# Optimization experiments

Measured on AMD Instinct MI355X. Metric: run time of the kernel, lower is better.

The kernel has to match this reference:

```python
import jax, jax.numpy as jnp
import numpy as np

N = 5000        # nodes (repo uses 'sample/5000')
D_IN = 512      # feature dim
D_OUT = 16      # output_dim
K = 3           # num meta-paths
N_CLASSES = 100 # num_Labels
P_EDGE = 0.0064 # ~32 avg degree


def setup_inputs() -> dict:
    key = jax.random.key(0)
    ks = jax.random.split(key, 8)
    features = jax.random.normal(ks[0], (N, D_IN), dtype=jnp.float32)
    # sparse binary similarity matrices, symmetrized
    adj = (jax.random.uniform(ks[1], (K, N, N)) < P_EDGE).astype(jnp.float32)
    adj = jnp.maximum(adj, adj.transpose(0, 2, 1))
    W_gnn = jax.random.normal(ks[2], (K, D_IN, D_OUT), dtype=jnp.float32) / np.sqrt(D_IN).astype(np.float32)
    b_gnn = jnp.zeros((K, D_OUT), dtype=jnp.float32)
    att_w = jax.random.normal(ks[3], (K, 2 * D_OUT, 1), dtype=jnp.float32)  # as in torch.randn
    W_final = jax.random.normal(ks[4], (D_OUT, N_CLASSES), dtype=jnp.float32) / np.sqrt(D_OUT).astype(np.float32)
    b_final = jnp.zeros((N_CLASSES,), dtype=jnp.float32)
    return dict(features=features, adj=adj, W_gnn=W_gnn, b_gnn=b_gnn,
                att_w=att_w, W_final=W_final, b_final=b_final)


def _gcn_norm(A_bin):
    # GCNConv normalization: D^{-1/2} (A + I) D^{-1/2} with unit edge weights
    n = A_bin.shape[-1]
    Ahat = A_bin + jnp.eye(n, dtype=A_bin.dtype)
    dinv = jax.lax.rsqrt(Ahat.sum(-1))  # deg >= 1 due to self loops
    return dinv[..., :, None] * Ahat * dinv[..., None, :]


def reference(features, adj, W_gnn, b_gnn, att_w, W_final, b_final):
    # --- per-meta-path GCNConv (edge weights are all 1, from nonzero pattern) ---
    norm = _gcn_norm((adj != 0).astype(features.dtype))          # [K,N,N]
    XW = jnp.einsum('nd,kdo->kno', features, W_gnn)              # [K,N,Dout]
    h = jnp.einsum('knm,kmo->kno', norm, XW) + b_gnn[:, None, :]
    f_meta = jnp.max(h, axis=0)                                  # 'max' aggregation, [N,Dout]

    # --- pairwise attention over meta-paths (vectorized NxN loop) ---
    d = f_meta.shape[1]
    a = f_meta @ att_w[:, :d, 0].T   # [N,K] contribution of f_meta[i]
    b = f_meta @ att_w[:, d:, 0].T   # [N,K] contribution of f_meta[j]
    scores = jnp.exp(jax.nn.relu(a[:, None, :] + b[None, :, :]))  # [N,N,K]
    attn = scores / scores.sum(-1, keepdims=True)

    # --- fuse meta-path adjacencies ---
    A_meta = jnp.einsum('nmk,knm->nm', attn, adj)                # [N,N]

    # --- final GCNConv on the nonzero pattern of A_meta (unit edge weights) ---
    norm_meta = _gcn_norm((A_meta != 0).astype(features.dtype))
    predictions = norm_meta @ (f_meta @ W_final) + b_final
    return f_meta, A_meta, predictions
```

## Files before the change

kernel.cpp:

```cpp
#include <hip/hip_runtime.h>
#include <cstdint>
#include <cstddef>

#define N_NODES 5000
#define DIN 512
#define DOUT 16
#define KMP 3
#define NCLS 100
#define WSTRIDE 160
#define NWORDS 157
#define NQ 1250
#define CAPK 160
#define CAPU 320
#define NJT 313
#define NXW (KMP * NJT)

typedef float f32x4 __attribute__((ext_vector_type(4)));

__global__ __launch_bounds__(256)
void kA(const float* __restrict__ adj, const float* __restrict__ feat,
        const float* __restrict__ Wg,
        uint32_t* __restrict__ planes, float* __restrict__ dinv,
        float* __restrict__ udinv,
        uint16_t* __restrict__ nbrK, int* __restrict__ cntK,
        uint16_t* __restrict__ nbrU, int* __restrict__ cntU,
        float* __restrict__ XW) {
    int bid = blockIdx.x;
    int t = threadIdx.x;

    if (bid >= N_NODES) {
        int b2 = bid - N_NODES;
        int k = b2 / NJT;
        int jt = b2 - k * NJT;
        int j = jt * 16 + (t >> 4);
        int o = t & 15;
        if (j < N_NODES) {
            const float4* f4 = (const float4*)(feat + (size_t)j * DIN);
            const float* wk = Wg + (size_t)k * DIN * DOUT + o;
            float acc = 0.f;
            #pragma unroll 4
            for (int d4 = 0; d4 < DIN / 4; ++d4) {
                float4 f = f4[d4];
                acc += f.x * wk[(4 * d4 + 0) * DOUT]
                     + f.y * wk[(4 * d4 + 1) * DOUT]
                     + f.z * wk[(4 * d4 + 2) * DOUT]
                     + f.w * wk[(4 * d4 + 3) * DOUT];
            }
            XW[((size_t)k * N_NODES + j) * DOUT + o] = acc;
        }
        return;
    }

    int i = bid;
    int lane = t & 63;
    int wv   = t >> 6;
    __shared__ uint32_t nib32[KMP][320];
    __shared__ int wtot[4][4];

    #pragma unroll
    for (int it = 0; it < 15; ++it) {
        const int k  = it / 5;
        const int ql = (it - 5 * k) * 256 + t;
        uint32_t m = 0;
        if (ql < NQ) {
            const f32x4* arow4 = (const f32x4*)(adj + ((size_t)k * N_NODES + i) * N_NODES);
            f32x4 v = __builtin_nontemporal_load(arow4 + ql);
            m = (v.x != 0.f ? 1u : 0u) | (v.y != 0.f ? 2u : 0u) |
                (v.z != 0.f ? 4u : 0u) | (v.w != 0.f ? 8u : 0u);
        }
        ((uint8_t*)nib32[k])[ql] = (uint8_t)m;
    }
    __syncthreads();

    uint32_t w[4];
    int cnt[4];
    #pragma unroll
    for (int k = 0; k < KMP; ++k) {
        uint32_t word = 0;
        if (t < NWORDS) {
            uint32_t lo = nib32[k][2 * t], hi = nib32[k][2 * t + 1];
            word = (lo & 0xFu) | ((lo >> 4) & 0xF0u) | ((lo >> 8) & 0xF00u) | ((lo >> 12) & 0xF000u)
                 | ((hi << 16) & 0xF0000u) | ((hi << 12) & 0xF00000u)
                 | ((hi << 8) & 0xF000000u) | ((hi << 4) & 0xF0000000u);
            planes[((size_t)k * N_NODES + i) * WSTRIDE + t] = word;
        }
        w[k] = word;
        cnt[k] = __popc(word);
    }
    w[3] = w[0] | w[1] | w[2];
    cnt[3] = __popc(w[3]);

    int x[4];
    #pragma unroll
    for (int q = 0; q < 4; ++q) x[q] = cnt[q];
    #pragma unroll
    for (int s = 1; s < 64; s <<= 1) {
        int y0 = __shfl_up(x[0], s), y1 = __shfl_up(x[1], s);
        int y2 = __shfl_up(x[2], s), y3 = __shfl_up(x[3], s);
        if (lane >= s) { x[0] += y0; x[1] += y1; x[2] += y2; x[3] += y3; }
    }
    if (lane == 63) {
        wtot[0][wv] = x[0]; wtot[1][wv] = x[1];
        wtot[2][wv] = x[2]; wtot[3][wv] = x[3];
    }
    __syncthreads();

    #pragma unroll
    for (int q = 0; q < 4; ++q) {
        int prefix = 0, total = 0;
        #pragma unroll
        for (int wq = 0; wq < 4; ++wq) {
            int v = wtot[q][wq];
            total += v;
            if (wq < wv) prefix += v;
        }
        int pos = prefix + x[q] - cnt[q];
        uint32_t word = w[q];
        if (q < KMP) {
            uint16_t* out = nbrK + ((size_t)q * N_NODES + i) * CAPK;
            while (word) {
                int b = __builtin_ctz(word);
                word &= word - 1;
                if (pos < CAPK) out[pos] = (uint16_t)(32 * t + b);
                ++pos;
            }
            if (t == 0) {
                dinv[q * N_NODES + i] = rsqrtf(1.0f + (float)total);
                cntK[q * N_NODES + i] = (total < CAPK) ? total : CAPK;
            }
        } else {
            uint16_t* out = nbrU + (size_t)i * CAPU;
            while (word) {
                int b = __builtin_ctz(word);
                word &= word - 1;
                if (pos < CAPU) out[pos] = (uint16_t)(32 * t + b);
                ++pos;
            }
            if (t == 0) {
                cntU[i] = (total < CAPU) ? total : CAPU;
                udinv[i] = rsqrtf(1.0f + (float)total);
            }
        }
    }
}

__global__ __launch_bounds__(256)
void k34_fmeta_ab_gd(const uint16_t* __restrict__ nbrK, const int* __restrict__ cntK,
                     const float* __restrict__ XW, const float* __restrict__ dinv,
                     const float* __restrict__ bg, const float* __restrict__ aw,
                     const float* __restrict__ Wf, const float* __restrict__ udinv,
                     float* __restrict__ f_meta, float* __restrict__ a4,
                     float* __restrict__ b4, float* __restrict__ Gd) {
    int t = threadIdx.x;
    int wv = t >> 6;
    int lane = t & 63;
    int o = lane & 15;
    int s = lane >> 4;
    int i = blockIdx.x * 4 + wv;
    __shared__ float fs[4][17];

    float hmax = -1e30f;
    #pragma unroll
    for (int k = 0; k < KMP; ++k) {
        const float* xw = XW + (size_t)k * N_NODES * DOUT;
        const float* dv = dinv + (size_t)k * N_NODES;
        int row = k * N_NODES + i;
        int nn = cntK[row];
        const uint16_t* nb = nbrK + (size_t)row * CAPK;
        float di = dv[i];
        float a0 = 0.f, a1 = 0.f, a2 = 0.f, a3 = 0.f;
        for (int n0 = 4 * s; n0 < nn; n0 += 16) {
            ushort4 jj = *(const ushort4*)(nb + n0);
            a0 += dv[jj.x] * xw[(int)jj.x * DOUT + o];
            if (n0 + 1 < nn) a1 += dv[jj.y] * xw[(int)jj.y * DOUT + o];
            if (n0 + 2 < nn) a2 += dv[jj.z] * xw[(int)jj.z * DOUT + o];
            if (n0 + 3 < nn) a3 += dv[jj.w] * xw[(int)jj.w * DOUT + o];
        }
        float red = (a0 + a1) + (a2 + a3);
        red += __shfl_xor(red, 16);
        red += __shfl_xor(red, 32);
        red += di * xw[i * DOUT + o];
        float h = di * red + bg[k * DOUT + o];
        hmax = fmaxf(hmax, h);
    }
    if (s == 0) {
        f_meta[i * DOUT + o] = hmax;
        fs[wv][o] = hmax;
    }
    __syncthreads();

    float sa0 = hmax * aw[0 * 32 + o], sb0 = hmax * aw[0 * 32 + 16 + o];
    float sa1 = hmax * aw[1 * 32 + o], sb1 = hmax * aw[1 * 32 + 16 + o];
    float sa2 = hmax * aw[2 * 32 + o], sb2 = hmax * aw[2 * 32 + 16 + o];
    #pragma unroll
    for (int sh = 1; sh < 16; sh <<= 1) {
        sa0 += __shfl_xor(sa0, sh, 16); sb0 += __shfl_xor(sb0, sh, 16);
        sa1 += __shfl_xor(sa1, sh, 16); sb1 += __shfl_xor(sb1, sh, 16);
        sa2 += __shfl_xor(sa2, sh, 16); sb2 += __shfl_xor(sb2, sh, 16);
    }
    if (s == 0 && o < 4) {
        float sa = (o == 0) ? sa0 : (o == 1) ? sa1 : (o == 2) ? sa2 : 0.f;
        float sb = (o == 0) ? sb0 : (o == 1) ? sb1 : (o == 2) ? sb2 : 0.f;
        a4[i * 4 + o] = sa;
        b4[i * 4 + o] = sb;
    }

    float f[DOUT];
    #pragma unroll
    for (int q = 0; q < DOUT; ++q) f[q] = fs[wv][q];
    float ud = udinv[i];
    for (int c = lane; c < NCLS; c += 64) {
        float acc = 0.f;
        #pragma unroll
        for (int q = 0; q < DOUT; ++q) acc += f[q] * Wf[q * NCLS + c];
        Gd[(size_t)i * NCLS + c] = acc * ud;
    }
}

__device__ __forceinline__ float attn_frac(float x0, float x1, float x2,
                                           uint32_t b0, uint32_t b1, uint32_t b2) {
    float e0 = __expf(fmaxf(x0, 0.f));
    float e1 = __expf(fmaxf(x1, 0.f));
    float e2 = __expf(fmaxf(x2, 0.f));
    float num = (b0 ? e0 : 0.f) + (b1 ? e1 : 0.f) + (b2 ? e2 : 0.f);
    return __fdividef(num, e0 + e1 + e2);
}

#define NB_K5 625

__global__ __launch_bounds__(256)
void kC(const uint32_t* __restrict__ planes,
        const float* __restrict__ a4, const float* __restrict__ b4,
        float* __restrict__ Am,
        const uint16_t* __restrict__ nbrU, const int* __restrict__ cntU,
        const float* __restrict__ Gd, const float* __restrict__ udinv,
        const float* __restrict__ bf, float* __restrict__ pred) {
    int bid = blockIdx.x;
    int t = threadIdx.x;

    if (bid < NB_K5) {
        int i0 = bid * 8;
        __shared__ float a_s[8][3];
        if (t < 24) { int r = t / 3, k = t % 3; a_s[r][k] = a4[(i0 + r) * 4 + k]; }
        __syncthreads();
        for (int c = 0; c < 5; ++c) {
            int j4 = 4 * (t + 256 * c);
            if (j4 >= N_NODES) break;
            int w = j4 >> 5, sh = j4 & 31;
            const float4* bp = (const float4*)(b4 + (size_t)j4 * 4);
            float4 bj0 = bp[0], bj1 = bp[1], bj2 = bp[2], bj3 = bp[3];
            #pragma unroll
            for (int r = 0; r < 8; ++r) {
                int i = i0 + r;
                uint32_t q0 = planes[(size_t)i * WSTRIDE + w] >> sh;
                uint32_t q1 = planes[(size_t)(N_NODES + i) * WSTRIDE + w] >> sh;
                uint32_t q2 = planes[(size_t)(2 * N_NODES + i) * WSTRIDE + w] >> sh;
                uint32_t un = (q0 | q1 | q2) & 0xFu;
                f32x4 outv = (f32x4)(0.f);
                if (un) {
                    float A0 = a_s[r][0], A1 = a_s[r][1], A2 = a_s[r][2];
                    if (un & 1u) outv.x = attn_frac(A0 + bj0.x, A1 + bj0.y, A2 + bj0.z, q0 & 1u, q1 & 1u, q2 & 1u);
                    if (un & 2u) outv.y = attn_frac(A0 + bj1.x, A1 + bj1.y, A2 + bj1.z, q0 & 2u, q1 & 2u, q2 & 2u);
                    if (un & 4u) outv.z = attn_frac(A0 + bj2.x, A1 + bj2.y, A2 + bj2.z, q0 & 4u, q1 & 4u, q2 & 4u);
                    if (un & 8u) outv.w = attn_frac(A0 + bj3.x, A1 + bj3.y, A2 + bj3.z, q0 & 8u, q1 & 8u, q2 & 8u);
                }
                __builtin_nontemporal_store(outv, (f32x4*)(Am + (size_t)i * N_NODES + j4));
            }
        }
    } else {
        int b2 = bid - NB_K5;
        int i = b2 * 2 + (t >> 7);
        int c = t & 127;
        if (c >= NCLS) return;
        int nn = cntU[i];
        const uint16_t* nb = nbrU + (size_t)i * CAPU;
        float a0 = Gd[(size_t)i * NCLS + c];
        float a1 = 0.f, a2 = 0.f, a3 = 0.f;
        int n = 0;
        for (; n + 4 <= nn; n += 4) {
            ushort4 jj = *(const ushort4*)(nb + n);
            a0 += Gd[(size_t)jj.x * NCLS + c];
            a1 += Gd[(size_t)jj.y * NCLS + c];
            a2 += Gd[(size_t)jj.z * NCLS + c];
            a3 += Gd[(size_t)jj.w * NCLS + c];
        }
        for (; n < nn; ++n) a0 += Gd[(size_t)nb[n] * NCLS + c];
        pred[(size_t)i * NCLS + c] = udinv[i] * ((a0 + a1) + (a2 + a3)) + bf[c];
    }
}

extern "C" void kernel_launch(void* const* d_in, const int* in_sizes, int n_in,
                              void* d_out, int out_size, void* d_ws, size_t ws_size,
                              hipStream_t stream) {
    const float* feat = (const float*)d_in[0];
    const float* adj  = (const float*)d_in[1];
    const float* Wg   = (const float*)d_in[2];
    const float* bg   = (const float*)d_in[3];
    const float* aw   = (const float*)d_in[4];
    const float* Wf   = (const float*)d_in[5];
    const float* bf   = (const float*)d_in[6];

    float* f_meta = (float*)d_out;
    float* Am     = f_meta + (size_t)N_NODES * DOUT;
    float* pred   = Am + (size_t)N_NODES * N_NODES;

    char* ws = (char*)d_ws;
    size_t off = 0;
    auto alloc = [&](size_t bytes) {
        void* p = ws + off;
        off = (off + bytes + 255) & ~(size_t)255;
        return p;
    };
    uint32_t* planes = (uint32_t*)alloc((size_t)KMP * N_NODES * WSTRIDE * 4);
    float* dinv  = (float*)alloc((size_t)KMP * N_NODES * 4);
    float* XW    = (float*)alloc((size_t)KMP * N_NODES * DOUT * 4);
    float* a4    = (float*)alloc((size_t)N_NODES * 16);
    float* b4    = (float*)alloc((size_t)N_NODES * 16);
    float* udinv = (float*)alloc((size_t)N_NODES * 4);
    float* Gd    = (float*)alloc((size_t)N_NODES * NCLS * 4);
    uint16_t* nbrK = (uint16_t*)alloc((size_t)KMP * N_NODES * CAPK * 2);
    int*      cntK = (int*)alloc((size_t)KMP * N_NODES * 4);
    uint16_t* nbrU = (uint16_t*)alloc((size_t)N_NODES * CAPU * 2);
    int*      cntU = (int*)alloc((size_t)N_NODES * 4);

    hipLaunchKernelGGL(kA, dim3(N_NODES + NXW), dim3(256), 0, stream,
                       adj, feat, Wg, planes, dinv, udinv, nbrK, cntK, nbrU, cntU, XW);
    hipLaunchKernelGGL(k34_fmeta_ab_gd, dim3(N_NODES / 4), dim3(256), 0, stream,
                       nbrK, cntK, XW, dinv, bg, aw, Wf, udinv, f_meta, a4, b4, Gd);
    hipLaunchKernelGGL(kC, dim3(NB_K5 + N_NODES / 2), dim3(256), 0, stream,
                       planes, a4, b4, Am, nbrU, cntU, Gd, udinv, bf, pred);
}
```

Baseline: 532.1 us.

## Rebalance work splits across XW, f_meta and A_meta kernels

The XW projection blocks now compute all three meta-paths per block, so each feature row is loaded once instead of three times, and the XW grid is a third the size. The f_meta kernel now uses one block per node with one wave per meta-path, combining results through shared memory instead of looping over meta-paths serially in a single wave. The A_meta kernel processes 4 rows per block instead of 8, doubling the block count. These changes trade redundant loads and serial loops for more parallelism, at the cost of extra blocks and more b4 reloads in the attention kernel.

```diff
diff --git a/kernel.cpp b/kernel.cpp
--- a/kernel.cpp
+++ b/kernel.cpp
@@ -13,7 +13,6 @@
 #define CAPK 160
 #define CAPU 320
 #define NJT 313
-#define NXW (KMP * NJT)
 
 typedef float f32x4 __attribute__((ext_vector_type(4)));
 
@@ -30,23 +29,28 @@
 
     if (bid >= N_NODES) {
         int b2 = bid - N_NODES;
-        int k = b2 / NJT;
-        int jt = b2 - k * NJT;
-        int j = jt * 16 + (t >> 4);
+        int j = b2 * 16 + (t >> 4);
         int o = t & 15;
         if (j < N_NODES) {
-            const float4* f4 = (const float4*)(feat + (size_t)j * DIN);
-            const float* wk = Wg + (size_t)k * DIN * DOUT + o;
-            float acc = 0.f;
-            #pragma unroll 4
+            const f32x4* f4 = (const f32x4*)(feat + (size_t)j * DIN);
+            const float* w0 = Wg + (size_t)0 * DIN * DOUT + o;
+            const float* w1 = Wg + (size_t)1 * DIN * DOUT + o;
+            const float* w2 = Wg + (size_t)2 * DIN * DOUT + o;
+            float acc0 = 0.f, acc1 = 0.f, acc2 = 0.f;
+            #pragma unroll 2
             for (int d4 = 0; d4 < DIN / 4; ++d4) {
-                float4 f = f4[d4];
-                acc += f.x * wk[(4 * d4 + 0) * DOUT]
-                     + f.y * wk[(4 * d4 + 1) * DOUT]
-                     + f.z * wk[(4 * d4 + 2) * DOUT]
-                     + f.w * wk[(4 * d4 + 3) * DOUT];
-            }
-            XW[((size_t)k * N_NODES + j) * DOUT + o] = acc;
+                f32x4 f = f4[d4];
+                int d = 4 * d4;
+                acc0 += f.x * w0[(d + 0) * DOUT] + f.y * w0[(d + 1) * DOUT]
+                      + f.z * w0[(d + 2) * DOUT] + f.w * w0[(d + 3) * DOUT];
+                acc1 += f.x * w1[(d + 0) * DOUT] + f.y * w1[(d + 1) * DOUT]
+                      + f.z * w1[(d + 2) * DOUT] + f.w * w1[(d + 3) * DOUT];
+                acc2 += f.x * w2[(d + 0) * DOUT] + f.y * w2[(d + 1) * DOUT]
+                      + f.z * w2[(d + 2) * DOUT] + f.w * w2[(d + 3) * DOUT];
+            }
+            XW[((size_t)0 * N_NODES + j) * DOUT + o] = acc0;
+            XW[((size_t)1 * N_NODES + j) * DOUT + o] = acc1;
+            XW[((size_t)2 * N_NODES + j) * DOUT + o] = acc2;
         }
         return;
     }
@@ -144,76 +148,71 @@
     }
 }
 
-__global__ __launch_bounds__(256)
+__global__ __launch_bounds__(192)
 void k34_fmeta_ab_gd(const uint16_t* __restrict__ nbrK, const int* __restrict__ cntK,
                      const float* __restrict__ XW, const float* __restrict__ dinv,
                      const float* __restrict__ bg, const float* __restrict__ aw,
                      const float* __restrict__ Wf, const float* __restrict__ udinv,
                      float* __restrict__ f_meta, float* __restrict__ a4,
                      float* __restrict__ b4, float* __restrict__ Gd) {
+    int i = blockIdx.x;
     int t = threadIdx.x;
-    int wv = t >> 6;
+    int k = t >> 6;
     int lane = t & 63;
     int o = lane & 15;
     int s = lane >> 4;
-    int i = blockIdx.x * 4 + wv;
-    __shared__ float fs[4][17];
-
-    float hmax = -1e30f;
-    #pragma unroll
-    for (int k = 0; k < KMP; ++k) {
-        const float* xw = XW + (size_t)k * N_NODES * DOUT;
-        const float* dv = dinv + (size_t)k * N_NODES;
-        int row = k * N_NODES + i;
-        int nn = cntK[row];
-        const uint16_t* nb = nbrK + (size_t)row * CAPK;
-        float di = dv[i];
-        float a0 = 0.f, a1 = 0.f, a2 = 0.f, a3 = 0.f;
-        for (int n0 = 4 * s; n0 < nn; n0 += 16) {
-            ushort4 jj = *(const ushort4*)(nb + n0);
-            a0 += dv[jj.x] * xw[(int)jj.x * DOUT + o];
-            if (n0 + 1 < nn) a1 += dv[jj.y] * xw[(int)jj.y * DOUT + o];
-            if (n0 + 2 < nn) a2 += dv[jj.z] * xw[(int)jj.z * DOUT + o];
-            if (n0 + 3 < nn) a3 += dv[jj.w] * xw[(int)jj.w * DOUT + o];
-        }
-        float red = (a0 + a1) + (a2 + a3);
-        red += __shfl_xor(red, 16);
-        red += __shfl_xor(red, 32);
-        red += di * xw[i * DOUT + o];
-        float h = di * red + bg[k * DOUT + o];
-        hmax = fmaxf(hmax, h);
-    }
-    if (s == 0) {
-        f_meta[i * DOUT + o] = hmax;
-        fs[wv][o] = hmax;
-    }
+    __shared__ float hs[KMP][16];
+    __shared__ float fm[16];
+
+    const float* xw = XW + (size_t)k * N_NODES * DOUT;
+    const float* dv = dinv + (size_t)k * N_NODES;
+    int row = k * N_NODES + i;
+    int nn = cntK[row];
+    const uint16_t* nb = nbrK + (size_t)row * CAPK;
+    float di = dv[i];
+    float a0 = 0.f, a1 = 0.f, a2 = 0.f, a3 = 0.f;
+    for (int n0 = 4 * s; n0 < nn; n0 += 16) {
+        ushort4 jj = *(const ushort4*)(nb + n0);
+        a0 += dv[jj.x] * xw[(int)jj.x * DOUT + o];
+        if (n0 + 1 < nn) a1 += dv[jj.y] * xw[(int)jj.y * DOUT + o];
+        if (n0 + 2 < nn) a2 += dv[jj.z] * xw[(int)jj.z * DOUT + o];
+        if (n0 + 3 < nn) a3 += dv[jj.w] * xw[(int)jj.w * DOUT + o];
+    }
+    float red = (a0 + a1) + (a2 + a3);
+    red += __shfl_xor(red, 16);
+    red += __shfl_xor(red, 32);
+    red += di * xw[i * DOUT + o];
+    float h = di * red + bg[k * DOUT + o];
+    if (s == 0) hs[k][o] = h;
     __syncthreads();
 
-    float sa0 = hmax * aw[0 * 32 + o], sb0 = hmax * aw[0 * 32 + 16 + o];
-    float sa1 = hmax * aw[1 * 32 + o], sb1 = hmax * aw[1 * 32 + 16 + o];
-    float sa2 = hmax * aw[2 * 32 + o], sb2 = hmax * aw[2 * 32 + 16 + o];
-    #pragma unroll
-    for (int sh = 1; sh < 16; sh <<= 1) {
-        sa0 += __shfl_xor(sa0, sh, 16); sb0 += __shfl_xor(sb0, sh, 16);
-        sa1 += __shfl_xor(sa1, sh, 16); sb1 += __shfl_xor(sb1, sh, 16);
-        sa2 += __shfl_xor(sa2, sh, 16); sb2 += __shfl_xor(sb2, sh, 16);
-    }
-    if (s == 0 && o < 4) {
-        float sa = (o == 0) ? sa0 : (o == 1) ? sa1 : (o == 2) ? sa2 : 0.f;
-        float sb = (o == 0) ? sb0 : (o == 1) ? sb1 : (o == 2) ? sb2 : 0.f;
-        a4[i * 4 + o] = sa;
-        b4[i * 4 + o] = sb;
-    }
-
-    float f[DOUT];
-    #pragma unroll
-    for (int q = 0; q < DOUT; ++q) f[q] = fs[wv][q];
-    float ud = udinv[i];
-    for (int c = lane; c < NCLS; c += 64) {
+    if (k == 0) {
+        float hm = fmaxf(fmaxf(hs[0][o], hs[1][o]), hs[2][o]);
+        if (s == 0) { f_meta[i * DOUT + o] = hm; fm[o] = hm; }
+        float sa0 = hm * aw[0 * 32 + o], sb0 = hm * aw[0 * 32 + 16 + o];
+        float sa1 = hm * aw[1 * 32 + o], sb1 = hm * aw[1 * 32 + 16 + o];
+        float sa2 = hm * aw[2 * 32 + o], sb2 = hm * aw[2 * 32 + 16 + o];
+        #pragma unroll
+        for (int sh = 1; sh < 16; sh <<= 1) {
+            sa0 += __shfl_xor(sa0, sh, 16); sb0 += __shfl_xor(sb0, sh, 16);
+            sa1 += __shfl_xor(sa1, sh, 16); sb1 += __shfl_xor(sb1, sh, 16);
+            sa2 += __shfl_xor(sa2, sh, 16); sb2 += __shfl_xor(sb2, sh, 16);
+        }
+        if (s == 0 && o < 4) {
+            float sa = (o == 0) ? sa0 : (o == 1) ? sa1 : (o == 2) ? sa2 : 0.f;
+            float sb = (o == 0) ? sb0 : (o == 1) ? sb1 : (o == 2) ? sb2 : 0.f;
+            a4[i * 4 + o] = sa;
+            b4[i * 4 + o] = sb;
+        }
+    }
+    __syncthreads();
+
+    if (t < NCLS) {
+        float ud = udinv[i];
         float acc = 0.f;
         #pragma unroll
-        for (int q = 0; q < DOUT; ++q) acc += f[q] * Wf[q * NCLS + c];
-        Gd[(size_t)i * NCLS + c] = acc * ud;
+        for (int q = 0; q < DOUT; ++q) acc += fm[q] * Wf[q * NCLS + t];
+        Gd[(size_t)i * NCLS + t] = acc * ud;
     }
 }
 
@@ -226,7 +225,7 @@
     return __fdividef(num, e0 + e1 + e2);
 }
 
-#define NB_K5 625
+#define NB_K5 1250
 
 __global__ __launch_bounds__(256)
 void kC(const uint32_t* __restrict__ planes,
@@ -239,9 +238,9 @@
     int t = threadIdx.x;
 
     if (bid < NB_K5) {
-        int i0 = bid * 8;
-        __shared__ float a_s[8][3];
-        if (t < 24) { int r = t / 3, k = t % 3; a_s[r][k] = a4[(i0 + r) * 4 + k]; }
+        int i0 = bid * 4;
+        __shared__ float a_s[4][3];
+        if (t < 12) { int r = t / 3, k = t % 3; a_s[r][k] = a4[(i0 + r) * 4 + k]; }
         __syncthreads();
         for (int c = 0; c < 5; ++c) {
             int j4 = 4 * (t + 256 * c);
@@ -250,7 +249,7 @@
             const float4* bp = (const float4*)(b4 + (size_t)j4 * 4);
             float4 bj0 = bp[0], bj1 = bp[1], bj2 = bp[2], bj3 = bp[3];
             #pragma unroll
-            for (int r = 0; r < 8; ++r) {
+            for (int r = 0; r < 4; ++r) {
                 int i = i0 + r;
                 uint32_t q0 = planes[(size_t)i * WSTRIDE + w] >> sh;
                 uint32_t q1 = planes[(size_t)(N_NODES + i) * WSTRIDE + w] >> sh;
@@ -323,9 +322,9 @@
     uint16_t* nbrU = (uint16_t*)alloc((size_t)N_NODES * CAPU * 2);
     int*      cntU = (int*)alloc((size_t)N_NODES * 4);
 
-    hipLaunchKernelGGL(kA, dim3(N_NODES + NXW), dim3(256), 0, stream,
+    hipLaunchKernelGGL(kA, dim3(N_NODES + NJT), dim3(256), 0, stream,
                        adj, feat, Wg, planes, dinv, udinv, nbrK, cntK, nbrU, cntU, XW);
-    hipLaunchKernelGGL(k34_fmeta_ab_gd, dim3(N_NODES / 4), dim3(256), 0, stream,
+    hipLaunchKernelGGL(k34_fmeta_ab_gd, dim3(N_NODES), dim3(192), 0, stream,
                        nbrK, cntK, XW, dinv, bg, aw, Wf, udinv, f_meta, a4, b4, Gd);
     hipLaunchKernelGGL(kC, dim3(NB_K5 + N_NODES / 2), dim3(256), 0, stream,
                        planes, a4, b4, Am, nbrU, cntU, Gd, udinv, bf, pred);
```

Result: no change. 536.4 us (+0.8%).
